# Kernel optimization log

Measured on AMD Instinct MI355X. Metric: run time of the kernel, lower is better.

Reference implementation:

```python
import jax, jax.numpy as jnp
import numpy as np

L, H, P = 16384, 1024, 512  # seq len, model width, state size (conj_sym: P = ssm_size//2)
DT_MIN, DT_MAX = 1e-3, 1e-1
STEP_RESCALE = 1.0


def setup_inputs() -> dict:
    key = jax.random.key(0)
    ks = jax.random.split(key, 7)
    input_sequence = jax.random.normal(ks[0], (L, H), dtype=jnp.float32)
    # Lambda: stable diagonal (Re < 0), like DPLR-HiPPO (Re = -0.5, spread imag parts)
    Lambda_re = -0.5 - jax.random.uniform(ks[1], (P,), dtype=jnp.float32)
    Lambda_im = 10.0 * jax.random.normal(ks[2], (P,), dtype=jnp.float32)
    # B (P,H,2) and C (H,P,2): real/imag stacked parameterization
    B = jax.random.normal(ks[3], (P, H, 2), dtype=jnp.float32) / np.float32(np.sqrt(H))
    C = jax.random.normal(ks[4], (H, P, 2), dtype=jnp.float32) / np.float32(np.sqrt(P))
    D = jax.random.normal(ks[5], (H,), dtype=jnp.float32)
    log_step = (jax.random.uniform(ks[6], (P, 1), dtype=jnp.float32)
                * (np.log(DT_MAX) - np.log(DT_MIN)) + np.log(DT_MIN)).astype(jnp.float32)
    return {"input_sequence": input_sequence, "Lambda_re": Lambda_re,
            "Lambda_im": Lambda_im, "B": B, "C": C, "D": D, "log_step": log_step}


def _binop(q_i, q_j):
    # diagonal linear recurrence composition; elementwise, so works on stacked arrays
    A_i, b_i = q_i
    A_j, b_j = q_j
    return (A_j * A_i, A_j * b_i + b_j)


def reference(input_sequence, Lambda_re, Lambda_im, B, C, D, log_step):
    Lambda = Lambda_re + 1j * Lambda_im                      # (P,) complex64
    B_tilde = B[..., 0] + 1j * B[..., 1]                     # (P,H)
    C_tilde = C[..., 0] + 1j * C[..., 1]                     # (H,P)
    Delta = STEP_RESCALE * jnp.exp(log_step[:, 0])           # (P,)
    # ZOH discretization
    Lambda_bar = jnp.exp(Lambda * Delta)                     # (P,)
    B_bar = ((Lambda_bar - 1.0) / Lambda)[:, None] * B_tilde # (P,H)
    # per-step scan elements
    Lambda_elements = jnp.broadcast_to(Lambda_bar, (input_sequence.shape[0], P))
    Bu_elements = jnp.einsum('lh,ph->lp', input_sequence, B_bar)  # (L,P) complex
    _, xs = jax.lax.associative_scan(_binop, (Lambda_elements, Bu_elements))
    # conj_sym readout: 2 * Re(C x)
    ys = 2.0 * jnp.einsum('lp,hp->lh', xs, C_tilde).real     # (L,H) float32
    return ys + input_sequence * D
```

## Files before the change

kernel.cpp:

```cpp
#include <hip/hip_runtime.h>
#include <math.h>

#define LL 16384
#define HH 1024
#define PP 512
#define NP2 1024
#define CHUNK 64
#define NCHUNK 256

#define BM2 128
#define BN2 256
#define SUBK 32
#define REG_U16 12288

typedef unsigned short u16;
typedef __attribute__((ext_vector_type(8))) short bf16x8;
typedef __attribute__((ext_vector_type(4))) float f32x4;

__device__ __forceinline__ u16 f2bf(float f) {
    unsigned u = __float_as_uint(f);
    unsigned r = 0x7fffu + ((u >> 16) & 1u);
    return (u16)((u + r) >> 16);
}
__device__ __forceinline__ float bf2f(u16 x) {
    return __uint_as_float(((unsigned)x) << 16);
}

__device__ __forceinline__ void gload_lds16(const void* g, void* l) {
    __builtin_amdgcn_global_load_lds(
        (const __attribute__((address_space(1))) unsigned int*)g,
        (__attribute__((address_space(3))) unsigned int*)l, 16, 0, 0);
}

#define SB0 __builtin_amdgcn_sched_barrier(0)

__global__ __launch_bounds__(256) void k_prep(
        const float* __restrict__ B, const float* __restrict__ C,
        const float* __restrict__ u, const float* __restrict__ lre,
        const float* __restrict__ lim, const float* __restrict__ logstep,
        u16* __restrict__ bb, u16* __restrict__ cp, u16* __restrict__ ub,
        float* __restrict__ lbre, float* __restrict__ lbim,
        float* __restrict__ ltre, float* __restrict__ ltim) {
    const int bx = blockIdx.x;
    if (bx < 2048) {
        int t = bx * 256 + threadIdx.x;
        int p = t >> 10, h = t & 1023;
        float2 b = ((const float2*)B)[t];
        float dt = expf(logstep[p]);
        float ar = lre[p], ai = lim[p];
        float e = expf(ar * dt);
        float s, c;
        sincosf(ai * dt, &s, &c);
        float nr = e * c - 1.0f, ni = e * s;
        float den = ar * ar + ai * ai;
        float gr = (nr * ar + ni * ai) / den;
        float gi = (ni * ar - nr * ai) / den;
        bb[(size_t)(2 * p) * HH + h]     = f2bf(gr * b.x - gi * b.y);
        bb[(size_t)(2 * p + 1) * HH + h] = f2bf(gr * b.y + gi * b.x);
    } else if (bx < 4096) {
        int t = (bx - 2048) * 256 + threadIdx.x;
        int h = t >> 9, p = t & 511;
        float2 c = ((const float2*)C)[t];
        cp[(size_t)h * NP2 + 2 * p]     = f2bf(c.x);
        cp[(size_t)h * NP2 + 2 * p + 1] = f2bf(-c.y);
    } else if (bx < 6144) {
        size_t base = ((size_t)(bx - 4096) * 256 + threadIdx.x) * 4;
        #pragma unroll
        for (int k = 0; k < 8; k++) {
            size_t i = base + (size_t)k * (2048 * 256 * 4);
            float4 v = *(const float4*)&u[i];
            unsigned lo = (unsigned)f2bf(v.x) | ((unsigned)f2bf(v.y) << 16);
            unsigned hi = (unsigned)f2bf(v.z) | ((unsigned)f2bf(v.w) << 16);
            *(uint2*)&ub[i] = make_uint2(lo, hi);
        }
    } else {
        int p = (bx - 6144) * 256 + threadIdx.x;
        if (p < PP) {
            float dt = expf(logstep[p]);
            float ar = lre[p], ai = lim[p];
            float e = expf(ar * dt);
            float s, c;
            sincosf(ai * dt, &s, &c);
            float Lr = e * c, Li = e * s;
            lbre[p] = Lr; lbim[p] = Li;
            float tr = Lr, ti = Li;
            for (int i6 = 0; i6 < 6; i6++) {
                float rr = tr * tr - ti * ti;
                float mm = 2.0f * tr * ti;
                tr = rr; ti = mm;
            }
            ltre[p] = tr; ltim[p] = ti;
        }
    }
}

template<int FUSE>
__global__ __launch_bounds__(512, 4) void k_gemm2(
        const u16* __restrict__ A, const u16* __restrict__ Bt,
        void* __restrict__ outp, const int K,
        const u16* __restrict__ ubf, const float* __restrict__ Din,
        const float* __restrict__ lbre, const float* __restrict__ lbim,
        float* __restrict__ frO, float* __restrict__ fiO) {
    extern __shared__ u16 smem[];
    const int b = blockIdx.x;
    const int xcd = b & 7, sidx = b >> 3;
    const int m0 = (xcd * 16 + (sidx >> 2)) * BM2;
    const int n0 = (sidx & 3) * BN2;
    const int t = threadIdx.x;
    const int lane = t & 63, wid = t >> 6;
    const int wm = (wid >> 2) * 64, wn = (wid & 3) * 64;
    const int frow = lane & 15, quad = (lane >> 4) & 3;

    f32x4 acc[4][4];
    #pragma unroll
    for (int i = 0; i < 4; i++)
        #pragma unroll
        for (int j = 0; j < 4; j++) acc[i][j] = (f32x4){0.f, 0.f, 0.f, 0.f};

    const int sr = t >> 2, slot = t & 3;
    const int seg = slot ^ ((sr >> 1) & 3);
    const u16* gA = A + (size_t)(m0 + sr) * K + seg * 8;
    const u16* gB = Bt + (size_t)(n0 + sr) * K + seg * 8;
    const int ldstA = sr * 32 + slot * 8;
    const int ldstB = 4096 + sr * 32 + slot * 8;

    const int aoff = (wm + frow) * 32 + ((quad ^ ((frow >> 1) & 3)) * 8);
    const int boff = 4096 + (wn + frow) * 32 + ((quad ^ ((frow >> 1) & 3)) * 8);

    const int NT = K / SUBK;

#define STAGE(slot_, k_) do {                                            \
        u16* dst_ = smem + (slot_) * REG_U16;                            \
        const u16* ga_ = gA + (size_t)(k_) * SUBK;                       \
        const u16* gb_ = gB + (size_t)(k_) * SUBK;                       \
        gload_lds16(ga_,                   dst_ + ldstA);                \
        gload_lds16(gb_,                   dst_ + ldstB);                \
        gload_lds16(gb_ + (size_t)128 * K, dst_ + ldstB + 4096);         \
    } while (0)

    STAGE(0, 0);
    STAGE(1, 1);
    asm volatile("s_waitcnt vmcnt(3)" ::: "memory");
    SB0;
    __builtin_amdgcn_s_barrier();
    SB0;

    int rc = 0;
    int rs = 2;
    for (int s = 0; s < NT; ++s) {
        const u16* R = smem + rc * REG_U16;
        bf16x8 av0 = *(const bf16x8*)&R[aoff + 0 * 512];
        bf16x8 av1 = *(const bf16x8*)&R[aoff + 1 * 512];
        bf16x8 av2 = *(const bf16x8*)&R[aoff + 2 * 512];
        bf16x8 av3 = *(const bf16x8*)&R[aoff + 3 * 512];
        bf16x8 bv0 = *(const bf16x8*)&R[boff + 0 * 512];
        bf16x8 bv1 = *(const bf16x8*)&R[boff + 1 * 512];
        bf16x8 bv2 = *(const bf16x8*)&R[boff + 2 * 512];
        bf16x8 bv3 = *(const bf16x8*)&R[boff + 3 * 512];
        if (s + 2 < NT) STAGE(rs, s + 2);
        SB0;
        __builtin_amdgcn_s_barrier();
        asm volatile("s_waitcnt lgkmcnt(0)" ::: "memory");
        SB0;
        __builtin_amdgcn_s_setprio(1);
        acc[0][0] = __builtin_amdgcn_mfma_f32_16x16x32_bf16(av0, bv0, acc[0][0], 0, 0, 0);
        acc[0][1] = __builtin_amdgcn_mfma_f32_16x16x32_bf16(av0, bv1, acc[0][1], 0, 0, 0);
        acc[0][2] = __builtin_amdgcn_mfma_f32_16x16x32_bf16(av0, bv2, acc[0][2], 0, 0, 0);
        acc[0][3] = __builtin_amdgcn_mfma_f32_16x16x32_bf16(av0, bv3, acc[0][3], 0, 0, 0);
        acc[1][0] = __builtin_amdgcn_mfma_f32_16x16x32_bf16(av1, bv0, acc[1][0], 0, 0, 0);
        acc[1][1] = __builtin_amdgcn_mfma_f32_16x16x32_bf16(av1, bv1, acc[1][1], 0, 0, 0);
        acc[1][2] = __builtin_amdgcn_mfma_f32_16x16x32_bf16(av1, bv2, acc[1][2], 0, 0, 0);
        acc[1][3] = __builtin_amdgcn_mfma_f32_16x16x32_bf16(av1, bv3, acc[1][3], 0, 0, 0);
        acc[2][0] = __builtin_amdgcn_mfma_f32_16x16x32_bf16(av2, bv0, acc[2][0], 0, 0, 0);
        acc[2][1] = __builtin_amdgcn_mfma_f32_16x16x32_bf16(av2, bv1, acc[2][1], 0, 0, 0);
        acc[2][2] = __builtin_amdgcn_mfma_f32_16x16x32_bf16(av2, bv2, acc[2][2], 0, 0, 0);
        acc[2][3] = __builtin_amdgcn_mfma_f32_16x16x32_bf16(av2, bv3, acc[2][3], 0, 0, 0);
        acc[3][0] = __builtin_amdgcn_mfma_f32_16x16x32_bf16(av3, bv0, acc[3][0], 0, 0, 0);
        acc[3][1] = __builtin_amdgcn_mfma_f32_16x16x32_bf16(av3, bv1, acc[3][1], 0, 0, 0);
        acc[3][2] = __builtin_amdgcn_mfma_f32_16x16x32_bf16(av3, bv2, acc[3][2], 0, 0, 0);
        acc[3][3] = __builtin_amdgcn_mfma_f32_16x16x32_bf16(av3, bv3, acc[3][3], 0, 0, 0);
        __builtin_amdgcn_s_setprio(0);
        if (s < NT - 2)       asm volatile("s_waitcnt vmcnt(3)" ::: "memory");
        else if (s == NT - 2) asm volatile("s_waitcnt vmcnt(0)" ::: "memory");
        SB0;
        __builtin_amdgcn_s_barrier();
        SB0;

        rc = (rc == 2) ? 0 : rc + 1;
        rs = (rs == 2) ? 0 : rs + 1;
    }
#undef STAGE

    if (FUSE) {
        float* smf = (float*)smem;
        float* Cout = (float*)outp;
        #pragma unroll
        for (int h = 0; h < 2; h++) {
            if ((wid >> 2) == h) {
                #pragma unroll
                for (int i = 0; i < 4; i++)
                    #pragma unroll
                    for (int j = 0; j < 4; j++) {
                        f32x4 v = acc[i][j];
                        #pragma unroll
                        for (int r = 0; r < 4; r++)
                            smf[(i * 16 + quad * 4 + r) * 256 + wn + j * 16 + frow]
                                = v[r];
                    }
            }
            __syncthreads();
            #pragma unroll
            for (int k = 0; k < 8; k++) {
                const int l = t + k * 512;
                const int row = l >> 6, c4 = (l & 63) * 4;
                const size_t o = (size_t)(m0 + h * 64 + row) * 1024 + n0 + c4;
                float4 s4 = ((const float4*)smf)[l];
                uint2 uv = *(const uint2*)&ubf[o];
                float4 dv = *(const float4*)&Din[n0 + c4];
                float4 r4;
                r4.x = 2.0f * s4.x + bf2f((u16)(uv.x & 0xffff)) * dv.x;
                r4.y = 2.0f * s4.y + bf2f((u16)(uv.x >> 16))    * dv.y;
                r4.z = 2.0f * s4.z + bf2f((u16)(uv.y & 0xffff)) * dv.z;
                r4.w = 2.0f * s4.w + bf2f((u16)(uv.y >> 16))    * dv.w;
                *(float4*)&Cout[o] = r4;
            }
            __syncthreads();
        }
    } else {
        u16* Cb = (u16*)outp;
        unsigned* sm32 = (unsigned*)smem;
        #pragma unroll
        for (int i = 0; i < 4; i++)
            #pragma unroll
            for (int j = 0; j < 4; j++) {
                f32x4 v = acc[i][j];
                #pragma unroll
                for (int r = 0; r < 4; r++)
                    smem[(wm + i * 16 + quad * 4 + r) * 256 + wn + j * 16 + frow]
                        = f2bf(v[r]);
            }
        __syncthreads();
        #pragma unroll
        for (int k = 0; k < 8; k++) {
            const int l = t + k * 512;
            const int row = l >> 5, c16 = (l & 31) * 8;
            *(uint4*)&Cb[(size_t)(m0 + row) * 1024 + n0 + c16] =
                ((const uint4*)smem)[l];
        }
        if (t < 256) {
            const int ch = t >> 7, q = t & 127;
            const int sp = (n0 >> 1) + q;
            const float sar = lbre[sp], sai = lbim[sp];
            float xr = 0.f, xi = 0.f;
            #pragma unroll 8
            for (int r = 0; r < 64; r++) {
                unsigned v = sm32[(ch * 64 + r) * 128 + q];
                float br = bf2f((u16)(v & 0xffff));
                float bi = bf2f((u16)(v >> 16));
                float nr = sar * xr - sai * xi + br;
                float ni = sar * xi + sai * xr + bi;
                xr = nr; xi = ni;
            }
            frO[((m0 >> 6) + ch) * PP + sp] = xr;
            fiO[((m0 >> 6) + ch) * PP + sp] = xi;
        }
    }
}

__global__ __launch_bounds__(256) void k_scan2(
        const float* __restrict__ fr, const float* __restrict__ fi,
        const float* __restrict__ ltre, const float* __restrict__ ltim,
        float* __restrict__ cr, float* __restrict__ ci) {
    __shared__ float Ar[NCHUNK], Ai[NCHUNK], br[NCHUNK], bi[NCHUNK];
    const int p = blockIdx.x;
    const int c = threadIdx.x;
    const float lr = ltre[p], li = ltim[p];
    Ar[c] = lr; Ai[c] = li;
    br[c] = fr[c * PP + p];
    bi[c] = fi[c * PP + p];
    __syncthreads();
    #pragma unroll
    for (int d = 1; d < NCHUNK; d <<= 1) {
        float pAr = 0.f, pAi = 0.f, pbr = 0.f, pbi = 0.f;
        const bool has = (c >= d);
        if (has) { pAr = Ar[c-d]; pAi = Ai[c-d]; pbr = br[c-d]; pbi = bi[c-d]; }
        float cAr = Ar[c], cAi = Ai[c], cbr = br[c], cbi = bi[c];
        __syncthreads();
        if (has) {
            Ar[c] = cAr * pAr - cAi * pAi;
            Ai[c] = cAr * pAi + cAi * pAr;
            br[c] = cAr * pbr - cAi * pbi + cbr;
            bi[c] = cAr * pbi + cAi * pbr + cbi;
        }
        __syncthreads();
    }
    cr[c * PP + p] = (c == 0) ? 0.f : br[c-1];
    ci[c * PP + p] = (c == 0) ? 0.f : bi[c-1];
}

__global__ void k_scan3(unsigned* __restrict__ bu,
                        const float* __restrict__ lbre, const float* __restrict__ lbim,
                        const float* __restrict__ cr, const float* __restrict__ ci) {
    int p = blockIdx.x * 256 + threadIdx.x;
    int c = blockIdx.y;
    float ar = lbre[p], ai = lbim[p];
    float xr = cr[c * PP + p], xi = ci[c * PP + p];
    unsigned* b = bu + (size_t)c * CHUNK * PP + p;
    for (int j = 0; j < CHUNK; j += 8) {
        unsigned vv[8];
        #pragma unroll
        for (int q = 0; q < 8; q++) vv[q] = b[q * PP];
        unsigned w[8];
        #pragma unroll
        for (int q = 0; q < 8; q++) {
            float br = bf2f((u16)(vv[q] & 0xffff));
            float bi = bf2f((u16)(vv[q] >> 16));
            float nr = ar * xr - ai * xi + br;
            float ni = ar * xi + ai * xr + bi;
            xr = nr; xi = ni;
            w[q] = (unsigned)f2bf(xr) | ((unsigned)f2bf(xi) << 16);
        }
        #pragma unroll
        for (int q = 0; q < 8; q++) b[q * PP] = w[q];
        b += 8 * PP;
    }
}

extern "C" void kernel_launch(void* const* d_in, const int* in_sizes, int n_in,
                              void* d_out, int out_size, void* d_ws, size_t ws_size,
                              hipStream_t stream) {
    const float* u       = (const float*)d_in[0];
    const float* lre     = (const float*)d_in[1];
    const float* lim     = (const float*)d_in[2];
    const float* B       = (const float*)d_in[3];
    const float* C       = (const float*)d_in[4];
    const float* D       = (const float*)d_in[5];
    const float* logstep = (const float*)d_in[6];
    float* out = (float*)d_out;

    float* w = (float*)d_ws;
    float* lbre = w + 1024;
    float* lbim = w + 1536;
    float* ltre = w + 2048;
    float* ltim = w + 2560;
    float* fr   = w + 4096;
    float* fi   = fr + NCHUNK * PP;
    float* cr   = fi + NCHUNK * PP;
    float* ci   = cr + NCHUNK * PP;
    u16*   bub  = (u16*)(w + (1 << 20));
    u16*   ub   = bub + (size_t)LL * NP2;
    u16*   bb   = ub + (size_t)LL * HH;
    u16*   cp   = bb + (size_t)NP2 * HH;

    static int attr_done = 0;
    if (!attr_done) {
        hipFuncSetAttribute(reinterpret_cast<const void*>(k_gemm2<0>),
                            hipFuncAttributeMaxDynamicSharedMemorySize, 73728);
        hipFuncSetAttribute(reinterpret_cast<const void*>(k_gemm2<1>),
                            hipFuncAttributeMaxDynamicSharedMemorySize, 73728);
        attr_done = 1;
    }

    k_prep<<<6146, 256, 0, stream>>>(B, C, u, lre, lim, logstep,
                                     bb, cp, ub, lbre, lbim, ltre, ltim);
    k_gemm2<0><<<(NP2 / BN2) * (LL / BM2), 512, 73728, stream>>>(
        ub, bb, bub, HH, nullptr, nullptr, lbre, lbim, fr, fi);
    k_scan2<<<PP, NCHUNK, 0, stream>>>(fr, fi, ltre, ltim, cr, ci);
    k_scan3<<<dim3(PP / 256, NCHUNK), 256, 0, stream>>>(
        (unsigned*)bub, lbre, lbim, cr, ci);
    k_gemm2<1><<<(HH / BN2) * (LL / BM2), 512, 73728, stream>>>(
        bub, cp, out, NP2, ub, D, nullptr, nullptr, nullptr, nullptr);
}
```

Baseline: 231.3 us.

## Switch GEMM to double-buffered LDS and split epilogues to raise occupancy

The GEMM main loop goes from a triple-buffered to a double-buffered LDS pipeline, with a full vmcnt(0) wait each step, which cuts dynamic shared memory from 72 KB to 48 KB. The epilogues are restaged in smaller pieces (quarter tiles for the fused fp32 output, half tiles for the bf16 output and chunk scan) so they fit in the smaller LDS. Launch bounds go from 4 to 6 blocks per CU to trade pipeline depth for more resident blocks. The risk is more exposed global-load latency per K step and extra barriers in the epilogue.

```diff
diff --git a/kernel.cpp b/kernel.cpp
--- a/kernel.cpp
+++ b/kernel.cpp
@@ -95,7 +95,7 @@
 }
 
 template<int FUSE>
-__global__ __launch_bounds__(512, 4) void k_gemm2(
+__global__ __launch_bounds__(512, 6) void k_gemm2(
         const u16* __restrict__ A, const u16* __restrict__ Bt,
         void* __restrict__ outp, const int K,
         const u16* __restrict__ ubf, const float* __restrict__ Din,
@@ -139,16 +139,13 @@
     } while (0)
 
     STAGE(0, 0);
-    STAGE(1, 1);
-    asm volatile("s_waitcnt vmcnt(3)" ::: "memory");
+    asm volatile("s_waitcnt vmcnt(0)" ::: "memory");
     SB0;
     __builtin_amdgcn_s_barrier();
     SB0;
 
-    int rc = 0;
-    int rs = 2;
     for (int s = 0; s < NT; ++s) {
-        const u16* R = smem + rc * REG_U16;
+        const u16* R = smem + (s & 1) * REG_U16;
         bf16x8 av0 = *(const bf16x8*)&R[aoff + 0 * 512];
         bf16x8 av1 = *(const bf16x8*)&R[aoff + 1 * 512];
         bf16x8 av2 = *(const bf16x8*)&R[aoff + 2 * 512];
@@ -157,7 +154,7 @@
         bf16x8 bv1 = *(const bf16x8*)&R[boff + 1 * 512];
         bf16x8 bv2 = *(const bf16x8*)&R[boff + 2 * 512];
         bf16x8 bv3 = *(const bf16x8*)&R[boff + 3 * 512];
-        if (s + 2 < NT) STAGE(rs, s + 2);
+        if (s + 1 < NT) STAGE((s + 1) & 1, s + 1);
         SB0;
         __builtin_amdgcn_s_barrier();
         asm volatile("s_waitcnt lgkmcnt(0)" ::: "memory");
@@ -180,20 +177,53 @@
         acc[3][2] = __builtin_amdgcn_mfma_f32_16x16x32_bf16(av3, bv2, acc[3][2], 0, 0, 0);
         acc[3][3] = __builtin_amdgcn_mfma_f32_16x16x32_bf16(av3, bv3, acc[3][3], 0, 0, 0);
         __builtin_amdgcn_s_setprio(0);
-        if (s < NT - 2)       asm volatile("s_waitcnt vmcnt(3)" ::: "memory");
-        else if (s == NT - 2) asm volatile("s_waitcnt vmcnt(0)" ::: "memory");
+        if (s + 1 < NT) asm volatile("s_waitcnt vmcnt(0)" ::: "memory");
         SB0;
         __builtin_amdgcn_s_barrier();
         SB0;
-
-        rc = (rc == 2) ? 0 : rc + 1;
-        rs = (rs == 2) ? 0 : rs + 1;
     }
 #undef STAGE
 
     if (FUSE) {
         float* smf = (float*)smem;
         float* Cout = (float*)outp;
+        #pragma unroll
+        for (int qp = 0; qp < 4; qp++) {
+            if ((wid >> 2) == (qp >> 1)) {
+                const int ib = (qp & 1) * 2;
+                #pragma unroll
+                for (int ii = 0; ii < 2; ii++) {
+                    #pragma unroll
+                    for (int j = 0; j < 4; j++) {
+                        f32x4 v = acc[ib + ii][j];
+                        #pragma unroll
+                        for (int r = 0; r < 4; r++)
+                            smf[(ii * 16 + quad * 4 + r) * 256 + wn + j * 16 + frow]
+                                = v[r];
+                    }
+                }
+            }
+            __syncthreads();
+            #pragma unroll
+            for (int k = 0; k < 4; k++) {
+                const int l = t + k * 512;
+                const int row = l >> 6, c4 = (l & 63) * 4;
+                const size_t o = (size_t)(m0 + qp * 32 + row) * 1024 + n0 + c4;
+                float4 s4 = ((const float4*)smf)[l];
+                uint2 uv = *(const uint2*)&ubf[o];
+                float4 dv = *(const float4*)&Din[n0 + c4];
+                float4 r4;
+                r4.x = 2.0f * s4.x + bf2f((u16)(uv.x & 0xffff)) * dv.x;
+                r4.y = 2.0f * s4.y + bf2f((u16)(uv.x >> 16))    * dv.y;
+                r4.z = 2.0f * s4.z + bf2f((u16)(uv.y & 0xffff)) * dv.z;
+                r4.w = 2.0f * s4.w + bf2f((u16)(uv.y >> 16))    * dv.w;
+                *(float4*)&Cout[o] = r4;
+            }
+            __syncthreads();
+        }
+    } else {
+        u16* Cb = (u16*)outp;
+        unsigned* sm32 = (unsigned*)smem;
         #pragma unroll
         for (int h = 0; h < 2; h++) {
             if ((wid >> 2) == h) {
@@ -204,65 +234,36 @@
                         f32x4 v = acc[i][j];
                         #pragma unroll
                         for (int r = 0; r < 4; r++)
-                            smf[(i * 16 + quad * 4 + r) * 256 + wn + j * 16 + frow]
-                                = v[r];
+                            smem[(i * 16 + quad * 4 + r) * 256 + wn + j * 16 + frow]
+                                = f2bf(v[r]);
                     }
             }
             __syncthreads();
             #pragma unroll
-            for (int k = 0; k < 8; k++) {
+            for (int k = 0; k < 4; k++) {
                 const int l = t + k * 512;
-                const int row = l >> 6, c4 = (l & 63) * 4;
-                const size_t o = (size_t)(m0 + h * 64 + row) * 1024 + n0 + c4;
-                float4 s4 = ((const float4*)smf)[l];
-                uint2 uv = *(const uint2*)&ubf[o];
-                float4 dv = *(const float4*)&Din[n0 + c4];
-                float4 r4;
-                r4.x = 2.0f * s4.x + bf2f((u16)(uv.x & 0xffff)) * dv.x;
-                r4.y = 2.0f * s4.y + bf2f((u16)(uv.x >> 16))    * dv.y;
-                r4.z = 2.0f * s4.z + bf2f((u16)(uv.y & 0xffff)) * dv.z;
-                r4.w = 2.0f * s4.w + bf2f((u16)(uv.y >> 16))    * dv.w;
-                *(float4*)&Cout[o] = r4;
+                const int row = l >> 5, c16 = (l & 31) * 8;
+                *(uint4*)&Cb[(size_t)(m0 + h * 64 + row) * 1024 + n0 + c16] =
+                    ((const uint4*)smem)[l];
+            }
+            if (t < 128) {
+                const int q = t;
+                const int sp = (n0 >> 1) + q;
+                const float sar = lbre[sp], sai = lbim[sp];
+                float xr = 0.f, xi = 0.f;
+                #pragma unroll 8
+                for (int r = 0; r < 64; r++) {
+                    unsigned v = sm32[r * 128 + q];
+                    float br = bf2f((u16)(v & 0xffff));
+                    float bi = bf2f((u16)(v >> 16));
+                    float nr = sar * xr - sai * xi + br;
+                    float ni = sar * xi + sai * xr + bi;
+                    xr = nr; xi = ni;
+                }
+                frO[((m0 >> 6) + h) * PP + sp] = xr;
+                fiO[((m0 >> 6) + h) * PP + sp] = xi;
             }
             __syncthreads();
-        }
-    } else {
-        u16* Cb = (u16*)outp;
-        unsigned* sm32 = (unsigned*)smem;
-        #pragma unroll
-        for (int i = 0; i < 4; i++)
-            #pragma unroll
-            for (int j = 0; j < 4; j++) {
-                f32x4 v = acc[i][j];
-                #pragma unroll
-                for (int r = 0; r < 4; r++)
-                    smem[(wm + i * 16 + quad * 4 + r) * 256 + wn + j * 16 + frow]
-                        = f2bf(v[r]);
-            }
-        __syncthreads();
-        #pragma unroll
-        for (int k = 0; k < 8; k++) {
-            const int l = t + k * 512;
-            const int row = l >> 5, c16 = (l & 31) * 8;
-            *(uint4*)&Cb[(size_t)(m0 + row) * 1024 + n0 + c16] =
-                ((const uint4*)smem)[l];
-        }
-        if (t < 256) {
-            const int ch = t >> 7, q = t & 127;
-            const int sp = (n0 >> 1) + q;
-            const float sar = lbre[sp], sai = lbim[sp];
-            float xr = 0.f, xi = 0.f;
-            #pragma unroll 8
-            for (int r = 0; r < 64; r++) {
-                unsigned v = sm32[(ch * 64 + r) * 128 + q];
-                float br = bf2f((u16)(v & 0xffff));
-                float bi = bf2f((u16)(v >> 16));
-                float nr = sar * xr - sai * xi + br;
-                float ni = sar * xi + sai * xr + bi;
-                xr = nr; xi = ni;
-            }
-            frO[((m0 >> 6) + ch) * PP + sp] = xr;
-            fiO[((m0 >> 6) + ch) * PP + sp] = xi;
         }
     }
 }
@@ -355,19 +356,19 @@
     static int attr_done = 0;
     if (!attr_done) {
         hipFuncSetAttribute(reinterpret_cast<const void*>(k_gemm2<0>),
-                            hipFuncAttributeMaxDynamicSharedMemorySize, 73728);
+                            hipFuncAttributeMaxDynamicSharedMemorySize, 49152);
         hipFuncSetAttribute(reinterpret_cast<const void*>(k_gemm2<1>),
-                            hipFuncAttributeMaxDynamicSharedMemorySize, 73728);
+                            hipFuncAttributeMaxDynamicSharedMemorySize, 49152);
         attr_done = 1;
     }
 
     k_prep<<<6146, 256, 0, stream>>>(B, C, u, lre, lim, logstep,
                                      bb, cp, ub, lbre, lbim, ltre, ltim);
-    k_gemm2<0><<<(NP2 / BN2) * (LL / BM2), 512, 73728, stream>>>(
+    k_gemm2<0><<<(NP2 / BN2) * (LL / BM2), 512, 49152, stream>>>(
         ub, bb, bub, HH, nullptr, nullptr, lbre, lbim, fr, fi);
     k_scan2<<<PP, NCHUNK, 0, stream>>>(fr, fi, ltre, ltim, cr, ci);
     k_scan3<<<dim3(PP / 256, NCHUNK), 256, 0, stream>>>(
         (unsigned*)bub, lbre, lbim, cr, ci);
-    k_gemm2<1><<<(HH / BN2) * (LL / BM2), 512, 73728, stream>>>(
+    k_gemm2<1><<<(HH / BN2) * (LL / BM2), 512, 49152, stream>>>(
         bub, cp, out, NP2, ub, D, nullptr, nullptr, nullptr, nullptr);
 }
```

New measurement: 747.1 us. 3.23x slower.
